# Performance work log

Measured on AMD Instinct MI355X. Metric: run time of the kernel, lower is better.

Reference implementation:

```python
import jax, jax.numpy as jnp
import numpy as np

INPUT_SIZE, OUTPUT_SIZE, HIDDEN, NUM_LAYERS, T = 32, 10, 1536, 2, 64


def _lstm_cell(x, h, c, W_ih, W_hh, b_ih, b_hh):
    # PyTorch LSTMCell: gates ordered i, f, g, o
    g = x @ W_ih.T + b_ih + h @ W_hh.T + b_hh
    i_, f_, g_, o_ = jnp.split(g, 4, axis=-1)
    c2 = jax.nn.sigmoid(f_) * c + jax.nn.sigmoid(i_) * jnp.tanh(g_)
    h2 = jax.nn.sigmoid(o_) * jnp.tanh(c2)
    return h2, c2


def setup_inputs() -> dict:
    key = jax.random.key(0)
    ks = jax.random.split(key, 16)
    s = 1.0 / np.sqrt(HIDDEN)
    u = lambda k, shape: jax.random.uniform(k, shape, jnp.float32, -s, s)
    return {
        "inputs": jax.random.normal(ks[0], (T, 1, INPUT_SIZE), jnp.float32),
        "h_init": jnp.zeros((NUM_LAYERS, 1, HIDDEN), jnp.float32),
        "c_init": jnp.zeros((NUM_LAYERS, 1, HIDDEN), jnp.float32),
        "W_ih0": u(ks[1], (4 * HIDDEN, INPUT_SIZE)),
        "W_hh0": u(ks[2], (4 * HIDDEN, HIDDEN)),
        "b_ih0": u(ks[3], (4 * HIDDEN,)),
        "b_hh0": u(ks[4], (4 * HIDDEN,)),
        "W_ih1": u(ks[5], (4 * HIDDEN, HIDDEN)),
        "W_hh1": u(ks[6], (4 * HIDDEN, HIDDEN)),
        "b_ih1": u(ks[7], (4 * HIDDEN,)),
        "b_hh1": u(ks[8], (4 * HIDDEN,)),
        "W_lin": u(ks[9], (OUTPUT_SIZE, HIDDEN)),
        "b_lin": u(ks[10], (OUTPUT_SIZE,)),
        "lookup": jnp.asarray(np.linspace(0.1, 1.0, OUTPUT_SIZE), jnp.float32),
    }


def reference(inputs, h_init, c_init, W_ih0, W_hh0, b_ih0, b_hh0,
              W_ih1, W_hh1, b_ih1, b_hh1, W_lin, b_lin, lookup):
    S = T * INPUT_SIZE  # total sequential sub-steps
    keys = jax.random.split(jax.random.key(42), S)
    iidx = jnp.arange(S) // INPUT_SIZE  # timestep index
    jidx = jnp.arange(S) % INPUT_SIZE   # feature sub-step index
    pos = jnp.arange(INPUT_SIZE)

    def step(carry, xs):
        h0, c0, h1, c1, x_aug = carry
        k, i, j = xs
        # fresh input at the start of each timestep (j == 0)
        x = jnp.where(j == 0, inputs[i], x_aug)  # [1, INPUT_SIZE]
        h0, c0 = _lstm_cell(x, h0, c0, W_ih0, W_hh0, b_ih0, b_hh0)
        h1, c1 = _lstm_cell(h0, h1, c1, W_ih1, W_hh1, b_ih1, b_hh1)
        logits = h1 @ W_lin.T + b_lin          # [1, OUTPUT_SIZE]
        probs = jax.nn.softmax(logits, -1)
        action = jax.random.categorical(k, logits, axis=-1)  # [1] int
        scale = jnp.where(j == 0, 1.0, lookup[action])        # [1]
        # mult: ones except position j scaled by lookup[action]
        new_x = x * jnp.where(pos[None, :] == j, scale[:, None], 1.0)
        return (h0, c0, h1, c1, new_x), (action, probs)

    carry0 = (h_init[0], c_init[0], h_init[1], c_init[1], inputs[0])
    _, (actions, probs) = jax.lax.scan(step, carry0, (keys, iidx, jidx))
    return actions, probs  # [S,1] int, [S,1,OUTPUT_SIZE] float
```

## Files before the change

kernel.cpp:

```cpp
#include <hip/hip_runtime.h>
#include <math.h>

#define NWG   256
#define TPB   512
#define H     1536
#define S_TOT 2048
#define RPW   6
#define GRW   24
#define OUTP  2048

#define SMEM_FLOATS (10 * H + 8 * H)
#define SMEM_BYTES  (SMEM_FLOATS * 4)

struct Params {
  const float* inputs; const float* h_init; const float* c_init;
  const float* W_ih0; const float* W_hh0; const float* b_ih0; const float* b_hh0;
  const float* W_ih1; const float* W_hh1; const float* b_ih1; const float* b_hh1;
  const float* W_lin; const float* b_lin; const float* lookup;
  float* out; float* h0g; float* h1g; unsigned* bar;
};

__device__ __forceinline__ float gload(const float* p) {
  return __hip_atomic_load(p, __ATOMIC_RELAXED, __HIP_MEMORY_SCOPE_AGENT);
}
__device__ __forceinline__ void gstore(float* p, float v) {
  __hip_atomic_store(p, v, __ATOMIC_RELAXED, __HIP_MEMORY_SCOPE_AGENT);
}

__device__ __forceinline__ void tf2x32(unsigned k0, unsigned k1,
                                       unsigned x0, unsigned x1,
                                       unsigned& o0, unsigned& o1) {
  unsigned ks2 = k0 ^ k1 ^ 0x1BD11BDAu;
  x0 += k0; x1 += k1;
#define TFR(r) { x0 += x1; x1 = ((x1 << r) | (x1 >> (32 - r))); x1 ^= x0; }
  TFR(13) TFR(15) TFR(26) TFR(6)   x0 += k1;  x1 += ks2 + 1u;
  TFR(17) TFR(29) TFR(16) TFR(24)  x0 += ks2; x1 += k0 + 2u;
  TFR(13) TFR(15) TFR(26) TFR(6)   x0 += k0;  x1 += k1 + 3u;
  TFR(17) TFR(29) TFR(16) TFR(24)  x0 += k1;  x1 += ks2 + 4u;
  TFR(13) TFR(15) TFR(26) TFR(6)   x0 += ks2; x1 += k0 + 5u;
#undef TFR
  o0 = x0; o1 = x1;
}

__device__ __forceinline__ double bsum64(double v) {
#pragma unroll
  for (int o = 32; o > 0; o >>= 1) v += __shfl_xor(v, o);
  return v;
}

__device__ __forceinline__ float sigf(float x) { return 1.0f / (1.0f + expf(-x)); }

__device__ __forceinline__ void flagbar(unsigned* bar, unsigned e, int tid, int wg) {
  __builtin_amdgcn_fence(__ATOMIC_RELEASE, "agent");
  __syncthreads();
  if (tid == 0)
    __hip_atomic_store(&bar[wg], e, __ATOMIC_RELEASE, __HIP_MEMORY_SCOPE_AGENT);
  if (tid < 64) {
    const unsigned* f = bar + tid * 4;
    bool done;
    do {
      int d0 = (int)(__hip_atomic_load(f + 0, __ATOMIC_RELAXED, __HIP_MEMORY_SCOPE_AGENT) - e);
      int d1 = (int)(__hip_atomic_load(f + 1, __ATOMIC_RELAXED, __HIP_MEMORY_SCOPE_AGENT) - e);
      int d2 = (int)(__hip_atomic_load(f + 2, __ATOMIC_RELAXED, __HIP_MEMORY_SCOPE_AGENT) - e);
      int d3 = (int)(__hip_atomic_load(f + 3, __ATOMIC_RELAXED, __HIP_MEMORY_SCOPE_AGENT) - e);
      done = ((d0 | d1 | d2 | d3) >= 0);
    } while (!__all(done));
    __builtin_amdgcn_fence(__ATOMIC_ACQUIRE, "agent");
  }
  __syncthreads();
}

__device__ __forceinline__ void cntbar(unsigned* cnt, unsigned target, int tid) {
  __builtin_amdgcn_fence(__ATOMIC_RELEASE, "agent");
  __syncthreads();
  if (tid == 0)
    (void)__hip_atomic_fetch_add(cnt, 1u, __ATOMIC_RELEASE, __HIP_MEMORY_SCOPE_AGENT);
  if (tid < 64) {
    for (;;) {
      unsigned c = __hip_atomic_load(cnt, __ATOMIC_RELAXED, __HIP_MEMORY_SCOPE_AGENT);
      if ((int)(c - target) >= 0) break;
      __builtin_amdgcn_s_sleep(4);
    }
    __builtin_amdgcn_fence(__ATOMIC_ACQUIRE, "agent");
  }
  __syncthreads();
}

__global__ __launch_bounds__(TPB, 1)
void lstm_persistent(Params P) {
  const int tid  = threadIdx.x;
  const int wg   = blockIdx.x;
  const int wv   = tid >> 6;
  const int lane = tid & 63;

  extern __shared__ float smem[];
  float* s_Wlin = smem;
  float* s_W3   = smem + 10 * H;

  __shared__ float s_Wih0[GRW * 32];
  __shared__ float s_h0[H], s_h1[H];
  __shared__ float s_bih0[GRW], s_bhh0[GRW], s_bih1[GRW], s_bhh1[GRW];
  __shared__ float s_hh1dot[GRW], s_gate[GRW];
  __shared__ float s_x[32];
  __shared__ float s_c0[RPW], s_c1[RPW];
  __shared__ float s_logits[16];
  __shared__ float s_blin[10], s_lookup[10];
  __shared__ int   s_action;

  unsigned* cnt = P.bar + 512;

  if (wg == 0 && tid == 0)
    __hip_atomic_store(cnt, 0u, __ATOMIC_RELAXED, __HIP_MEMORY_SCOPE_AGENT);
  for (int k = tid; k < GRW * 32; k += TPB) {
    int idx = k >> 5, kk = k & 31;
    int q = idx / RPW, u = idx % RPW;
    int gr = q * H + wg * RPW + u;
    s_Wih0[k] = P.W_ih0[gr * 32 + kk];
  }
  for (int k = tid; k < 10 * H; k += TPB) s_Wlin[k] = P.W_lin[k];
  for (int k = tid; k < 8 * H; k += TPB) {
    int w8 = k / H, col = k % H;
    int idx = w8 * 3 + 2;
    int q = idx / RPW, u = idx % RPW;
    int gr = q * H + wg * RPW + u;
    s_W3[k] = P.W_ih1[(size_t)gr * H + col];
  }
  if (tid < GRW) {
    int q = tid / RPW, u = tid % RPW;
    int gr = q * H + wg * RPW + u;
    s_bih0[tid] = P.b_ih0[gr]; s_bhh0[tid] = P.b_hh0[gr];
    s_bih1[tid] = P.b_ih1[gr]; s_bhh1[tid] = P.b_hh1[gr];
  }
  if (tid < 10) { s_blin[tid] = P.b_lin[tid]; s_lookup[tid] = P.lookup[tid]; }
  if (tid < RPW) {
    s_c0[tid] = P.c_init[wg * RPW + tid];
    s_c1[tid] = P.c_init[H + wg * RPW + tid];
    gstore(P.h0g + wg * RPW + tid, P.h_init[wg * RPW + tid]);
    gstore(P.h1g + wg * RPW + tid, P.h_init[H + wg * RPW + tid]);
  }

  float wr[8][24];
#pragma unroll
  for (int slot = 0; slot < 3; ++slot) {
    int idx = wv * 3 + slot;
    int q = idx / RPW, u = idx % RPW;
    int gr = q * H + wg * RPW + u;
    const float* r0 = P.W_hh0 + (size_t)gr * H;
    const float* r1 = P.W_hh1 + (size_t)gr * H;
#pragma unroll
    for (int t = 0; t < 24; ++t) {
      int off = lane + (t << 6);
      wr[slot][t] = r0[off]; wr[3 + slot][t] = r1[off];
    }
  }
#pragma unroll
  for (int slot = 0; slot < 2; ++slot) {
    int idx = wv * 3 + slot;
    int q = idx / RPW, u = idx % RPW;
    int gr = q * H + wg * RPW + u;
    const float* r2 = P.W_ih1 + (size_t)gr * H;
#pragma unroll
    for (int t = 0; t < 24; ++t) wr[6 + slot][t] = r2[lane + (t << 6)];
  }

  flagbar(P.bar, 1u, tid, wg);
  unsigned bt = 0;

  for (int s = 0; s <= S_TOT; ++s) {
#pragma unroll
    for (int r = 0; r < 3; ++r) {
      int k = tid + r * TPB;
      s_h0[k] = gload(P.h0g + k);
      s_h1[k] = gload(P.h1g + k);
    }
    __syncthreads();

    if (s > 0) {
      int sp = s - 1;
#pragma unroll
      for (int p2 = 0; p2 < 2; ++p2) {
        int l = wv + 8 * p2;
        if (l < 10) {
          double acc = 0.0;
#pragma unroll
          for (int t = 0; t < 24; ++t) {
            int off = lane + (t << 6);
            acc += (double)s_Wlin[l * H + off] * (double)s_h1[off];
          }
          acc = bsum64(acc);
          if (lane == 0) s_logits[l] = __fadd_rn((float)acc, s_blin[l]);
        }
      }
      __syncthreads();

      if (wv == 0) {
        unsigned kk0, kk1; tf2x32(0u, 42u, 0u, (unsigned)sp, kk0, kk1);
        unsigned b1, b2; tf2x32(kk0, kk1, 0u, (unsigned)lane, b1, b2);
        unsigned bits = b1 ^ b2;
        float uraw = __fsub_rn(__uint_as_float((bits >> 9) | 0x3F800000u), 1.0f);
        const float TINY = 1.17549435e-38f;
        float u  = fmaxf(TINY, __fadd_rn(uraw, TINY));
        float gum = -logf(-logf(u));
        float lg = (lane < 10) ? s_logits[lane] : 0.0f;
        float y  = (lane < 10) ? __fadd_rn(lg, gum) : -INFINITY;
        int ai = lane;
#pragma unroll
        for (int o = 1; o < 16; o <<= 1) {
          float oy = __shfl_xor(y, o); int oi = __shfl_xor(ai, o);
          if (oy > y || (oy == y && oi < ai)) { y = oy; ai = oi; }
        }
        float lm = (lane < 10) ? lg : -INFINITY;
#pragma unroll
        for (int o = 1; o < 16; o <<= 1) lm = fmaxf(lm, __shfl_xor(lm, o));
        float e2 = (lane < 10) ? expf(__fsub_rn(lg, lm)) : 0.0f;
        float ssum = e2;
#pragma unroll
        for (int o = 1; o < 16; o <<= 1) ssum = __fadd_rn(ssum, __shfl_xor(ssum, o));
        if (lane == 0) s_action = ai;
        if (wg == 0) {
          if (lane < 10) P.out[OUTP + sp * 10 + lane] = e2 / ssum;
          if (lane == 0) P.out[sp] = (float)ai;
        }
      }
      __syncthreads();
      if (tid == 0) {
        int jp = sp & 31;
        if (jp != 0) s_x[jp] = __fmul_rn(s_x[jp], s_lookup[s_action]);
      }
      __syncthreads();
    }

    if (s == S_TOT) break;
    int ii = s >> 5, jj = s & 31;
    if (jj == 0 && tid < 32) s_x[tid] = P.inputs[ii * 32 + tid];
    __syncthreads();

    {
      double a0 = 0, a1 = 0, a2 = 0, b0 = 0, b1 = 0, b2 = 0;
#pragma unroll
      for (int t = 0; t < 24; ++t) {
        int off = lane + (t << 6);
        double h0v = (double)s_h0[off];
        double h1v = (double)s_h1[off];
        a0 += (double)wr[0][t] * h0v;
        a1 += (double)wr[1][t] * h0v;
        a2 += (double)wr[2][t] * h0v;
        b0 += (double)wr[3][t] * h1v;
        b1 += (double)wr[4][t] * h1v;
        b2 += (double)wr[5][t] * h1v;
      }
      a0 = bsum64(a0); a1 = bsum64(a1); a2 = bsum64(a2);
      b0 = bsum64(b0); b1 = bsum64(b1); b2 = bsum64(b2);
      double xa[3];
#pragma unroll
      for (int slot = 0; slot < 3; ++slot) {
        int idx = wv * 3 + slot;
        double pp = (lane < 32)
          ? (double)s_Wih0[(idx << 5) + lane] * (double)s_x[lane] : 0.0;
#pragma unroll
        for (int o = 16; o > 0; o >>= 1) pp += __shfl_xor(pp, o);
        xa[slot] = pp;
      }
      if (lane == 0) {
        double aa[3] = {a0, a1, a2}, bb[3] = {b0, b1, b2};
#pragma unroll
        for (int slot = 0; slot < 3; ++slot) {
          int idx = wv * 3 + slot;
          float g0 = __fadd_rn(__fadd_rn(__fadd_rn((float)xa[slot], s_bih0[idx]),
                                         (float)aa[slot]), s_bhh0[idx]);
          s_gate[idx]   = g0;
          s_hh1dot[idx] = (float)bb[slot];
        }
      }
    }
    __syncthreads();
    if (tid < RPW) {
      int u = tid;
      float gi = s_gate[u], gf = s_gate[6 + u], gg = s_gate[12 + u], go = s_gate[18 + u];
      float c = __fadd_rn(__fmul_rn(sigf(gf), s_c0[u]), __fmul_rn(sigf(gi), tanhf(gg)));
      s_c0[u] = c;
      float h = __fmul_rn(sigf(go), tanhf(c));
      gstore(P.h0g + wg * RPW + u, h);
    }
    bt += NWG; cntbar(cnt, bt, tid);

#pragma unroll
    for (int r = 0; r < 3; ++r) {
      int k = tid + r * TPB;
      s_h0[k] = gload(P.h0g + k);
    }
    __syncthreads();
    {
      double a0 = 0, a1 = 0, a2 = 0;
#pragma unroll
      for (int t = 0; t < 24; ++t) {
        int off = lane + (t << 6);
        double hv = (double)s_h0[off];
        a0 += (double)wr[6][t] * hv;
        a1 += (double)wr[7][t] * hv;
        a2 += (double)s_W3[wv * H + off] * hv;
      }
      a0 = bsum64(a0); a1 = bsum64(a1); a2 = bsum64(a2);
      if (lane == 0) {
        double aa[3] = {a0, a1, a2};
#pragma unroll
        for (int slot = 0; slot < 3; ++slot) {
          int idx = wv * 3 + slot;
          s_gate[idx] = __fadd_rn(__fadd_rn(__fadd_rn((float)aa[slot], s_bih1[idx]),
                                            s_hh1dot[idx]), s_bhh1[idx]);
        }
      }
    }
    __syncthreads();
    if (tid < RPW) {
      int u = tid;
      float gi = s_gate[u], gf = s_gate[6 + u], gg = s_gate[12 + u], go = s_gate[18 + u];
      float c = __fadd_rn(__fmul_rn(sigf(gf), s_c1[u]), __fmul_rn(sigf(gi), tanhf(gg)));
      s_c1[u] = c;
      float h = __fmul_rn(sigf(go), tanhf(c));
      gstore(P.h1g + wg * RPW + u, h);
    }
    bt += NWG; cntbar(cnt, bt, tid);
  }
}

extern "C" void kernel_launch(void* const* d_in, const int* in_sizes, int n_in,
                              void* d_out, int out_size, void* d_ws, size_t ws_size,
                              hipStream_t stream) {
  (void)in_sizes; (void)n_in; (void)out_size; (void)ws_size;
  Params p;
  p.inputs = (const float*)d_in[0];
  p.h_init = (const float*)d_in[1];
  p.c_init = (const float*)d_in[2];
  p.W_ih0  = (const float*)d_in[3];
  p.W_hh0  = (const float*)d_in[4];
  p.b_ih0  = (const float*)d_in[5];
  p.b_hh0  = (const float*)d_in[6];
  p.W_ih1  = (const float*)d_in[7];
  p.W_hh1  = (const float*)d_in[8];
  p.b_ih1  = (const float*)d_in[9];
  p.b_hh1  = (const float*)d_in[10];
  p.W_lin  = (const float*)d_in[11];
  p.b_lin  = (const float*)d_in[12];
  p.lookup = (const float*)d_in[13];
  p.out    = (float*)d_out;
  float* ws = (float*)d_ws;
  p.h0g = ws;
  p.h1g = ws + H;
  p.bar = (unsigned*)(ws + 2 * H);

  hipFuncSetAttribute((const void*)lstm_persistent,
                      hipFuncAttributeMaxDynamicSharedMemorySize, SMEM_BYTES);
  hipLaunchKernelGGL(lstm_persistent, dim3(NWG), dim3(TPB), SMEM_BYTES, stream, p);
}
```

Before: 188.1 ms.

## Double workgroup size to 16 waves and split gate rows across waves

Raises threads per block from 512 to 1024 and re-partitions the per-workgroup gate rows so each wave handles either W_hh0 or W_hh1 rows, which halves the per-wave register-resident weights and the serial dot-product work. The layer-1 input projection is now one register row per wave, with the remaining 8 rows served from LDS by the first 8 waves. The intent is to shorten the latency-bound critical path of each sequential step through more parallelism per CU. The cost is more waves taking part in every __syncthreads and barrier, and uneven load because waves 0-7 do the extra LDS row and the input projection.

```diff
diff --git a/kernel.cpp b/kernel.cpp
--- a/kernel.cpp
+++ b/kernel.cpp
@@ -2,7 +2,7 @@
 #include <math.h>
 
 #define NWG   256
-#define TPB   512
+#define TPB   1024
 #define H     1536
 #define S_TOT 2048
 #define RPW   6
@@ -86,7 +86,7 @@
   __syncthreads();
 }
 
-__global__ __launch_bounds__(TPB, 1)
+__global__ __launch_bounds__(TPB)
 void lstm_persistent(Params P) {
   const int tid  = threadIdx.x;
   const int wg   = blockIdx.x;
@@ -119,8 +119,8 @@
   }
   for (int k = tid; k < 10 * H; k += TPB) s_Wlin[k] = P.W_lin[k];
   for (int k = tid; k < 8 * H; k += TPB) {
-    int w8 = k / H, col = k % H;
-    int idx = w8 * 3 + 2;
+    int r8 = k / H, col = k % H;
+    int idx = 16 + r8;
     int q = idx / RPW, u = idx % RPW;
     int gr = q * H + wg * RPW + u;
     s_W3[k] = P.W_ih1[(size_t)gr * H + col];
@@ -139,37 +139,33 @@
     gstore(P.h1g + wg * RPW + tid, P.h_init[H + wg * RPW + tid]);
   }
 
-  float wr[8][24];
-#pragma unroll
-  for (int slot = 0; slot < 3; ++slot) {
-    int idx = wv * 3 + slot;
-    int q = idx / RPW, u = idx % RPW;
-    int gr = q * H + wg * RPW + u;
-    const float* r0 = P.W_hh0 + (size_t)gr * H;
-    const float* r1 = P.W_hh1 + (size_t)gr * H;
-#pragma unroll
-    for (int t = 0; t < 24; ++t) {
-      int off = lane + (t << 6);
-      wr[slot][t] = r0[off]; wr[3 + slot][t] = r1[off];
-    }
-  }
-#pragma unroll
-  for (int slot = 0; slot < 2; ++slot) {
-    int idx = wv * 3 + slot;
+  float wrA[3][24];
+  float wrB[24];
+  {
+    const float* srcA = (wv < 8) ? P.W_hh0 : P.W_hh1;
+    int baseA = (wv < 8) ? wv * 3 : (wv - 8) * 3;
+#pragma unroll
+    for (int slot = 0; slot < 3; ++slot) {
+      int idx = baseA + slot;
+      int q = idx / RPW, u = idx % RPW;
+      int gr = q * H + wg * RPW + u;
+      const float* r0 = srcA + (size_t)gr * H;
+#pragma unroll
+      for (int t = 0; t < 24; ++t) wrA[slot][t] = r0[lane + (t << 6)];
+    }
+    int idx = wv;
     int q = idx / RPW, u = idx % RPW;
     int gr = q * H + wg * RPW + u;
     const float* r2 = P.W_ih1 + (size_t)gr * H;
 #pragma unroll
-    for (int t = 0; t < 24; ++t) wr[6 + slot][t] = r2[lane + (t << 6)];
+    for (int t = 0; t < 24; ++t) wrB[t] = r2[lane + (t << 6)];
   }
 
   flagbar(P.bar, 1u, tid, wg);
   unsigned bt = 0;
 
   for (int s = 0; s <= S_TOT; ++s) {
-#pragma unroll
-    for (int r = 0; r < 3; ++r) {
-      int k = tid + r * TPB;
+    for (int k = tid; k < H; k += TPB) {
       s_h0[k] = gload(P.h0g + k);
       s_h1[k] = gload(P.h1g + k);
     }
@@ -177,9 +173,8 @@
 
     if (s > 0) {
       int sp = s - 1;
-#pragma unroll
-      for (int p2 = 0; p2 < 2; ++p2) {
-        int l = wv + 8 * p2;
+      {
+        int l = wv;
         if (l < 10) {
           double acc = 0.0;
 #pragma unroll
@@ -236,40 +231,45 @@
     __syncthreads();
 
     {
-      double a0 = 0, a1 = 0, a2 = 0, b0 = 0, b1 = 0, b2 = 0;
+      const float* hp = (wv < 8) ? s_h0 : s_h1;
+      double a0 = 0, a1 = 0, a2 = 0;
 #pragma unroll
       for (int t = 0; t < 24; ++t) {
         int off = lane + (t << 6);
-        double h0v = (double)s_h0[off];
-        double h1v = (double)s_h1[off];
-        a0 += (double)wr[0][t] * h0v;
-        a1 += (double)wr[1][t] * h0v;
-        a2 += (double)wr[2][t] * h0v;
-        b0 += (double)wr[3][t] * h1v;
-        b1 += (double)wr[4][t] * h1v;
-        b2 += (double)wr[5][t] * h1v;
+        double hv = (double)hp[off];
+        a0 += (double)wrA[0][t] * hv;
+        a1 += (double)wrA[1][t] * hv;
+        a2 += (double)wrA[2][t] * hv;
       }
       a0 = bsum64(a0); a1 = bsum64(a1); a2 = bsum64(a2);
-      b0 = bsum64(b0); b1 = bsum64(b1); b2 = bsum64(b2);
-      double xa[3];
-#pragma unroll
-      for (int slot = 0; slot < 3; ++slot) {
-        int idx = wv * 3 + slot;
-        double pp = (lane < 32)
-          ? (double)s_Wih0[(idx << 5) + lane] * (double)s_x[lane] : 0.0;
-#pragma unroll
-        for (int o = 16; o > 0; o >>= 1) pp += __shfl_xor(pp, o);
-        xa[slot] = pp;
-      }
-      if (lane == 0) {
-        double aa[3] = {a0, a1, a2}, bb[3] = {b0, b1, b2};
+      if (wv < 8) {
+        double xa[3];
 #pragma unroll
         for (int slot = 0; slot < 3; ++slot) {
           int idx = wv * 3 + slot;
-          float g0 = __fadd_rn(__fadd_rn(__fadd_rn((float)xa[slot], s_bih0[idx]),
-                                         (float)aa[slot]), s_bhh0[idx]);
-          s_gate[idx]   = g0;
-          s_hh1dot[idx] = (float)bb[slot];
+          double pp = (lane < 32)
+            ? (double)s_Wih0[(idx << 5) + lane] * (double)s_x[lane] : 0.0;
+#pragma unroll
+          for (int o = 16; o > 0; o >>= 1) pp += __shfl_xor(pp, o);
+          xa[slot] = pp;
+        }
+        if (lane == 0) {
+          double aa[3] = {a0, a1, a2};
+#pragma unroll
+          for (int slot = 0; slot < 3; ++slot) {
+            int idx = wv * 3 + slot;
+            s_gate[idx] = __fadd_rn(__fadd_rn(__fadd_rn((float)xa[slot], s_bih0[idx]),
+                                              (float)aa[slot]), s_bhh0[idx]);
+          }
+        }
+      } else {
+        if (lane == 0) {
+          double aa[3] = {a0, a1, a2};
+#pragma unroll
+          for (int slot = 0; slot < 3; ++slot) {
+            int idx = (wv - 8) * 3 + slot;
+            s_hh1dot[idx] = (float)aa[slot];
+          }
         }
       }
     }
@@ -284,29 +284,34 @@
     }
     bt += NWG; cntbar(cnt, bt, tid);
 
-#pragma unroll
-    for (int r = 0; r < 3; ++r) {
-      int k = tid + r * TPB;
+    for (int k = tid; k < H; k += TPB) {
       s_h0[k] = gload(P.h0g + k);
     }
     __syncthreads();
     {
-      double a0 = 0, a1 = 0, a2 = 0;
+      double a0 = 0;
 #pragma unroll
       for (int t = 0; t < 24; ++t) {
         int off = lane + (t << 6);
-        double hv = (double)s_h0[off];
-        a0 += (double)wr[6][t] * hv;
-        a1 += (double)wr[7][t] * hv;
-        a2 += (double)s_W3[wv * H + off] * hv;
-      }
-      a0 = bsum64(a0); a1 = bsum64(a1); a2 = bsum64(a2);
+        a0 += (double)wrB[t] * (double)s_h0[off];
+      }
+      a0 = bsum64(a0);
       if (lane == 0) {
-        double aa[3] = {a0, a1, a2};
-#pragma unroll
-        for (int slot = 0; slot < 3; ++slot) {
-          int idx = wv * 3 + slot;
-          s_gate[idx] = __fadd_rn(__fadd_rn(__fadd_rn((float)aa[slot], s_bih1[idx]),
+        int idx = wv;
+        s_gate[idx] = __fadd_rn(__fadd_rn(__fadd_rn((float)a0, s_bih1[idx]),
+                                          s_hh1dot[idx]), s_bhh1[idx]);
+      }
+      if (wv < 8) {
+        double a1 = 0;
+#pragma unroll
+        for (int t = 0; t < 24; ++t) {
+          int off = lane + (t << 6);
+          a1 += (double)s_W3[wv * H + off] * (double)s_h0[off];
+        }
+        a1 = bsum64(a1);
+        if (lane == 0) {
+          int idx = 16 + wv;
+          s_gate[idx] = __fadd_rn(__fadd_rn(__fadd_rn((float)a1, s_bih1[idx]),
                                             s_hh1dot[idx]), s_bhh1[idx]);
         }
       }
```

Result: slower. 236.2 ms (+25.6%).
